# Kernel optimization log

Hardware: AMD Instinct MI355X
Metric: run time of the kernel (lower is better)

## Reference

```python
import jax, jax.numpy as jnp
import numpy as np

D_MODEL = 1024
NUM_HEADS = 16
DEPTH = D_MODEL // NUM_HEADS


def setup_inputs() -> dict:
    key = jax.random.key(0)
    ks = jax.random.split(key, 12)
    B, S = 4, 2048
    scale = 1.0 / np.sqrt(D_MODEL)
    inp = {
        "query": jax.random.normal(ks[0], (B, S, D_MODEL), jnp.float32),
        "key": jax.random.normal(ks[1], (B, S, D_MODEL), jnp.float32),
        "value": jax.random.normal(ks[2], (B, S, D_MODEL), jnp.float32),
        "mask": jnp.zeros((B, 1, 1, S), jnp.float32),  # 1.0 => masked position
        "wq": jax.random.normal(ks[3], (D_MODEL, D_MODEL), jnp.float32) * scale,
        "bq": jnp.zeros((D_MODEL,), jnp.float32),
        "wk": jax.random.normal(ks[4], (D_MODEL, D_MODEL), jnp.float32) * scale,
        "bk": jnp.zeros((D_MODEL,), jnp.float32),
        "wv": jax.random.normal(ks[5], (D_MODEL, D_MODEL), jnp.float32) * scale,
        "bv": jnp.zeros((D_MODEL,), jnp.float32),
        "wo": jax.random.normal(ks[6], (D_MODEL, D_MODEL), jnp.float32) * scale,
        "bo": jnp.zeros((D_MODEL,), jnp.float32),
    }
    return inp


def _split_heads(x, B):
    # (B, S, d_model) -> (B, H, S, depth)
    return x.reshape(B, -1, NUM_HEADS, DEPTH).transpose(0, 2, 1, 3)


def reference(query, key, value, mask, wq, bq, wk, bk, wv, bv, wo, bo):
    B, Sq, _ = query.shape
    q = _split_heads(query @ wq + bq, B)   # (B,H,Sq,dh)
    k = _split_heads(key @ wk + bk, B)     # (B,H,Sk,dh)
    v = _split_heads(value @ wv + bv, B)   # (B,H,Sk,dh)

    logits = jnp.einsum("bhqd,bhkd->bhqk", q, k) / jnp.sqrt(
        jnp.asarray(DEPTH, q.dtype))
    logits = logits + mask * (-1e9)
    attn = jax.nn.softmax(logits, axis=-1)
    ctx = jnp.einsum("bhqk,bhkd->bhqd", attn, v)
    ctx = ctx.transpose(0, 2, 1, 3).reshape(B, Sq, D_MODEL)
    return ctx @ wo + bo
```

## Files before the change

kernel.cpp:

```cpp
#include <hip/hip_runtime.h>
#include <stdint.h>


typedef unsigned short u16;
typedef __attribute__((ext_vector_type(8))) short bf16x8;
typedef __attribute__((ext_vector_type(4))) short bf16x4;
typedef __attribute__((ext_vector_type(4))) float f32x4;

#define LOG2E 1.4426950408889634f

__device__ __forceinline__ u16 f2bf(float f) {
  uint32_t u = __builtin_bit_cast(uint32_t, f);
  u += 0x7fffu + ((u >> 16) & 1u);
  return (u16)(u >> 16);
}
__device__ __forceinline__ uint32_t cvt_pk(float a, float b) {
  uint32_t r;
  asm("v_cvt_pk_bf16_f32 %0, %1, %2" : "=v"(r) : "v"(a), "v"(b));
  return r;
}
__device__ __forceinline__ void gload16(const u16* g, u16* l) {
  __builtin_amdgcn_global_load_lds(
      (const __attribute__((address_space(1))) uint32_t*)(const void*)g,
      (__attribute__((address_space(3))) uint32_t*)(void*)l, 16, 0, 0);
}
__device__ __forceinline__ f32x4 mfma16(bf16x4 a, bf16x4 b, f32x4 c) {
#if __has_builtin(__builtin_amdgcn_mfma_f32_16x16x16bf16_1k)
  return __builtin_amdgcn_mfma_f32_16x16x16bf16_1k(a, b, c, 0, 0, 0);
#else
  f32x4 d = c;
  asm volatile("v_mfma_f32_16x16x16_bf16 %0, %1, %2, %0"
               : "+v"(d) : "v"(a), "v"(b));
  return d;
#endif
}

__global__ __launch_bounds__(256) void convert_x(
    const float* __restrict__ X, u16* __restrict__ Xb)
{
  const size_t i = ((size_t)blockIdx.x * 256 + threadIdx.x) * 8;
  const float4 a = *(const float4*)(X + i);
  const float4 b = *(const float4*)(X + i + 4);
  uint4 o;
  o.x = cvt_pk(a.x, a.y); o.y = cvt_pk(a.z, a.w);
  o.z = cvt_pk(b.x, b.y); o.w = cvt_pk(b.z, b.w);
  *(uint4*)(Xb + i) = o;
}

__global__ __launch_bounds__(256) void prep_mask(
    const float* __restrict__ mask, float* __restrict__ M2)
{
  const int i = blockIdx.x * 256 + threadIdx.x;
  M2[i] = mask[i] * (-1.0e9f * LOG2E);
}

__global__ __launch_bounds__(256) void transpose_w(
    const float* __restrict__ W0, const float* __restrict__ W1,
    const float* __restrict__ W2, const float* __restrict__ W3,
    u16* __restrict__ Wt)
{
  const int z = blockIdx.z;
  const float* W = (z == 0) ? W0 : (z == 1) ? W1 : (z == 2) ? W2 : W3;
  u16* T = Wt + ((size_t)z << 20);
  const int n0 = blockIdx.x * 64, k0 = blockIdx.y * 64;
  const int tid = threadIdx.x;
  const int r = tid >> 4, c4 = (tid & 15) * 4;
  __shared__ float t[64][65];
#pragma unroll
  for (int j = 0; j < 4; ++j) {
    const int row = r + j * 16;
    const float4 v = *(const float4*)(W + (size_t)(k0 + row) * 1024 + n0 + c4);
    t[c4 + 0][row] = v.x; t[c4 + 1][row] = v.y;
    t[c4 + 2][row] = v.z; t[c4 + 3][row] = v.w;
  }
  __syncthreads();
#pragma unroll
  for (int j = 0; j < 4; ++j) {
    const int nrow = r + j * 16;
    uint2 o;
    o.x = cvt_pk(t[nrow][c4 + 0], t[nrow][c4 + 1]);
    o.y = cvt_pk(t[nrow][c4 + 2], t[nrow][c4 + 3]);
    *(uint2*)(T + (size_t)(n0 + nrow) * 1024 + k0 + c4) = o;
  }
}

__global__ __launch_bounds__(256) void gemm_proj(
    const u16* __restrict__ A, const u16* __restrict__ Wt,
    const float* __restrict__ Bi, u16* __restrict__ O16,
    float* __restrict__ O32, int mode)
{
  const int bid = blockIdx.x;
  const int nid = (bid & 7) * 64 + (bid >> 3);
  const int n0 = (nid & 7) * 128;
  const int m0 = (nid >> 3) * 128;
  const int tid = threadIdx.x;
  const int w = tid >> 6, l = tid & 63, lo = l & 15, hi = l >> 4;
  const int wr = w >> 1, wc = w & 1;

  __shared__ __align__(16) u16 As[128 * 32];
  __shared__ __align__(16) u16 Bs[128 * 32];

  const f32x4 fz = {0.f, 0.f, 0.f, 0.f};
  f32x4 acc[4][4];
#pragma unroll
  for (int m = 0; m < 4; ++m)
#pragma unroll
    for (int n = 0; n < 4; ++n) acc[m][n] = fz;

  const int srow = w * 32 + (l >> 2);
  const u16* ga = A  + (size_t)(m0 + srow) * 1024 + (l & 3) * 8;
  const u16* gb = Wt + (size_t)(n0 + srow) * 1024 + (l & 3) * 8;
  u16* lA0 = &As[w * 1024];  u16* lA1 = &As[w * 1024 + 512];
  u16* lB0 = &Bs[w * 1024];  u16* lB1 = &Bs[w * 1024 + 512];

  for (int k0 = 0; k0 < 1024; k0 += 32) {
    __syncthreads();
    gload16(ga,             lA0);
    gload16(ga + 16 * 1024, lA1);
    gload16(gb,             lB0);
    gload16(gb + 16 * 1024, lB1);
    ga += 32; gb += 32;
    __syncthreads();

    bf16x8 af[4], bf[4];
#pragma unroll
    for (int m = 0; m < 4; ++m)
      af[m] = *(const bf16x8*)&As[(wr * 64 + m * 16 + lo) * 32 + hi * 8];
#pragma unroll
    for (int n = 0; n < 4; ++n)
      bf[n] = *(const bf16x8*)&Bs[(wc * 64 + n * 16 + lo) * 32 + hi * 8];
#pragma unroll
    for (int m = 0; m < 4; ++m)
#pragma unroll
      for (int n = 0; n < 4; ++n)
        acc[m][n] = __builtin_amdgcn_mfma_f32_16x16x32_bf16(af[m], bf[n], acc[m][n], 0, 0, 0);
  }

#pragma unroll
  for (int m = 0; m < 4; ++m) {
#pragma unroll
    for (int n = 0; n < 4; ++n) {
      const int col = n0 + wc * 64 + n * 16 + lo;
      const float bc = Bi[col];
      const int h = col >> 6, d = col & 63;
#pragma unroll
      for (int i = 0; i < 4; ++i) {
        const int r = m0 + wr * 64 + m * 16 + hi * 4 + i;
        const int b = r >> 11, s = r & 2047;
        float v = acc[m][n][i] + bc;
        if (mode == 0) {
          v *= 0.125f * LOG2E;
          O16[((size_t)((b * 16 + h) * 2048 + s)) * 64 + d] = f2bf(v);
        } else if (mode == 1) {
          O16[((size_t)((b * 16 + h) * 2048 + s)) * 64 + d] = f2bf(v);
        } else if (mode == 2) {
          O16[((size_t)((b * 16 + h) * 64 + d)) * 2048 + s] = f2bf(v);
        } else {
          O32[(size_t)r * 1024 + col] = v;
        }
      }
    }
  }
}

__global__ __launch_bounds__(512, 4) void attn(
    const u16* __restrict__ Q, const u16* __restrict__ K,
    const u16* __restrict__ Vt, const float* __restrict__ M2,
    u16* __restrict__ Ctx)
{
  const int bid = blockIdx.x;
  const int nid = (bid & 7) * 128 + (bid >> 3);
  const int qt = nid & 15;
  const int bh = nid >> 4;
  const int b = bh >> 4, h = bh & 15;
  const int tid = threadIdx.x;
  const int w = tid >> 6, l = tid & 63, lo = l & 15, hi = l >> 4;

  __shared__ __align__(16) u16 Kl[2][64 * 64];
  __shared__ __align__(16) u16 Vl[2][64 * 64];
  __shared__ __align__(16) float Msk[2048];

  const u16* Qb = Q + (size_t)bh * (2048 * 64);
  const u16* Kb = K + (size_t)bh * (2048 * 64);
  const u16* Vb = Vt + (size_t)bh * (64 * 2048);

  *(float4*)&Msk[tid * 4] = *(const float4*)(M2 + (size_t)b * 2048 + tid * 4);

  const int qrow = qt * 128 + w * 16 + lo;
  const bf16x8 qa0 = *(const bf16x8*)(Qb + (size_t)qrow * 64 + hi * 8);
  const bf16x8 qa1 = *(const bf16x8*)(Qb + (size_t)qrow * 64 + 32 + hi * 8);

  const f32x4 fz = {0.f, 0.f, 0.f, 0.f};
  f32x4 o[4] = {fz, fz, fz, fz};
  f32x4 ol = fz;
  const short oneb = (short)0x3F80;
  const bf16x4 ones = {oneb, oneb, oneb, oneb};
  const int lo7 = lo & 7;

  const int row = tid >> 3;
  const int sl = (tid & 7) ^ (row & 7);
  const u16* gK = Kb + (size_t)row * 64 + sl * 8;
  const u16* gV = Vb + (size_t)row * 2048 + sl * 8;

#define STAGE(kt_, buf_)                                  \
  do {                                                    \
    gload16(gK + (size_t)(kt_) * 4096, &Kl[buf_][w * 512]); \
    gload16(gV + (kt_) * 64,           &Vl[buf_][w * 512]); \
  } while (0)

  STAGE(0, 0);
  __syncthreads();

  for (int kt = 0; kt < 32; ++kt) {
    const int cur = kt & 1;
    STAGE((kt + 1) & 31, cur ^ 1);
    asm volatile("s_waitcnt vmcnt(2)" ::: "memory");
    __builtin_amdgcn_s_barrier();

    const int kv0 = kt * 64;
    const u16* Kc = &Kl[cur][0];
    const u16* Vc = &Vl[cur][0];

    f32x4 st[4];
    __builtin_amdgcn_s_setprio(1);
#pragma unroll
    for (int f = 0; f < 4; ++f) {
      const int krow = (f * 16 + lo) * 64;
      const bf16x8 kb0 = *(const bf16x8*)&Kc[krow + ((hi ^ lo7) << 3)];
      const bf16x8 kb1 = *(const bf16x8*)&Kc[krow + (((4 + hi) ^ lo7) << 3)];
      const f32x4 c = *(const f32x4*)&Msk[kv0 + 16 * f + 4 * hi];
      f32x4 a = __builtin_amdgcn_mfma_f32_16x16x32_bf16(kb0, qa0, c, 0, 0, 0);
      st[f] = __builtin_amdgcn_mfma_f32_16x16x32_bf16(kb1, qa1, a, 0, 0, 0);
    }
    __builtin_amdgcn_s_setprio(0);

    union { uint32_t u[2]; bf16x4 v; } pa[4];
#pragma unroll
    for (int f = 0; f < 4; ++f) {
      const float p0 = exp2f(st[f][0]);
      const float p1 = exp2f(st[f][1]);
      const float p2 = exp2f(st[f][2]);
      const float p3 = exp2f(st[f][3]);
      pa[f].u[0] = cvt_pk(p0, p1);
      pa[f].u[1] = cvt_pk(p2, p3);
    }

    __builtin_amdgcn_s_setprio(1);
#pragma unroll
    for (int f = 0; f < 4; ++f) {
      ol = mfma16(pa[f].v, ones, ol);
#pragma unroll
      for (int nf = 0; nf < 4; ++nf) {
        const int vrow = (lo + 16 * nf) * 64;
        const int slot = (((2 * f + (hi >> 1)) ^ lo7) << 3) + ((hi & 1) << 2);
        const bf16x4 vb = *(const bf16x4*)&Vc[vrow + slot];
        o[nf] = mfma16(pa[f].v, vb, o[nf]);
      }
    }
    __builtin_amdgcn_s_setprio(0);

    asm volatile("s_waitcnt lgkmcnt(0)" ::: "memory");
    __builtin_amdgcn_s_barrier();
  }
#undef STAGE

  float invq[4];
#pragma unroll
  for (int i = 0; i < 4; ++i) invq[i] = 1.f / ol[i];
#pragma unroll
  for (int nf = 0; nf < 4; ++nf) {
#pragma unroll
    for (int i = 0; i < 4; ++i) {
      const int s = qt * 128 + w * 16 + hi * 4 + i;
      const int d = nf * 16 + lo;
      Ctx[((size_t)((b * 2048 + s) * 16 + h)) * 64 + d] = f2bf(o[nf][i] * invq[i]);
    }
  }
}

extern "C" void kernel_launch(void* const* d_in, const int* in_sizes, int n_in,
                              void* d_out, int out_size, void* d_ws, size_t ws_size,
                              hipStream_t stream) {
  const float* q_in = (const float*)d_in[0];
  const float* k_in = (const float*)d_in[1];
  const float* v_in = (const float*)d_in[2];
  const float* mask = (const float*)d_in[3];
  const float* wq = (const float*)d_in[4];
  const float* bq = (const float*)d_in[5];
  const float* wk = (const float*)d_in[6];
  const float* bk = (const float*)d_in[7];
  const float* wv = (const float*)d_in[8];
  const float* bv = (const float*)d_in[9];
  const float* wo = (const float*)d_in[10];
  const float* bo = (const float*)d_in[11];

  u16* ws  = (u16*)d_ws;
  u16* wtq = ws;
  u16* wtk = wtq + (1u << 20);
  u16* wtv = wtk + (1u << 20);
  u16* wto = wtv + (1u << 20);
  u16* Qb  = wto + (1u << 20);
  u16* Kb  = Qb + (size_t)8192 * 1024;
  u16* Vtb = Kb + (size_t)8192 * 1024;
  u16* xbf = Vtb + (size_t)8192 * 1024;
  u16* ctx = xbf;
  float* M2 = (float*)(xbf + (size_t)8192 * 1024);

  transpose_w<<<dim3(16, 16, 4), 256, 0, stream>>>(wq, wk, wv, wo, wtq);
  prep_mask<<<32, 256, 0, stream>>>(mask, M2);

  convert_x<<<4096, 256, 0, stream>>>(q_in, xbf);
  gemm_proj<<<512, 256, 0, stream>>>(xbf, wtq, bq, Qb, nullptr, 0);
  convert_x<<<4096, 256, 0, stream>>>(k_in, xbf);
  gemm_proj<<<512, 256, 0, stream>>>(xbf, wtk, bk, Kb, nullptr, 1);
  convert_x<<<4096, 256, 0, stream>>>(v_in, xbf);
  gemm_proj<<<512, 256, 0, stream>>>(xbf, wtv, bv, Vtb, nullptr, 2);

  attn<<<1024, 512, 0, stream>>>(Qb, Kb, Vtb, M2, ctx);

  gemm_proj<<<512, 256, 0, stream>>>(ctx, wto, bo, nullptr, (float*)d_out, 3);
}
```

Baseline: 281.2 us.

## Process two query row-tiles per wave in attention with 256-thread blocks

The attention kernel drops from 8 waves to 4 waves per block, and each wave now handles 32 query rows as two 16-row MFMA tiles. Each K/V fragment read from LDS is therefore reused across two tiles, which halves LDS read traffic per unit of MFMA work. Each thread now issues twice as many staging loads and holds twice as many accumulators. The cost is higher register pressure and fewer waves per block to hide latency.

Result: faster. 268.5 us (-4.5%).

```diff
diff --git a/kernel.cpp b/kernel.cpp
--- a/kernel.cpp
+++ b/kernel.cpp
@@ -163,7 +163,7 @@
   }
 }
 
-__global__ __launch_bounds__(512, 4) void attn(
+__global__ __launch_bounds__(256, 4) void attn(
     const u16* __restrict__ Q, const u16* __restrict__ K,
     const u16* __restrict__ Vt, const float* __restrict__ M2,
     u16* __restrict__ Ctx)
@@ -176,36 +176,48 @@
   const int tid = threadIdx.x;
   const int w = tid >> 6, l = tid & 63, lo = l & 15, hi = l >> 4;
 
-  __shared__ __align__(16) u16 Kl[2][64 * 64];
-  __shared__ __align__(16) u16 Vl[2][64 * 64];
+  __shared__ __align__(16) u16 Kl[2][4096];
+  __shared__ __align__(16) u16 Vl[2][4096];
   __shared__ __align__(16) float Msk[2048];
 
   const u16* Qb = Q + (size_t)bh * (2048 * 64);
   const u16* Kb = K + (size_t)bh * (2048 * 64);
   const u16* Vb = Vt + (size_t)bh * (64 * 2048);
 
-  *(float4*)&Msk[tid * 4] = *(const float4*)(M2 + (size_t)b * 2048 + tid * 4);
-
-  const int qrow = qt * 128 + w * 16 + lo;
-  const bf16x8 qa0 = *(const bf16x8*)(Qb + (size_t)qrow * 64 + hi * 8);
-  const bf16x8 qa1 = *(const bf16x8*)(Qb + (size_t)qrow * 64 + 32 + hi * 8);
+  {
+    const float* ms = M2 + (size_t)b * 2048 + tid * 8;
+    *(float4*)&Msk[tid * 8]     = *(const float4*)(ms);
+    *(float4*)&Msk[tid * 8 + 4] = *(const float4*)(ms + 4);
+  }
+
+  const int qrow0 = qt * 128 + w * 32 + lo;
+  const bf16x8 qa00 = *(const bf16x8*)(Qb + (size_t)qrow0 * 64 + hi * 8);
+  const bf16x8 qa01 = *(const bf16x8*)(Qb + (size_t)qrow0 * 64 + 32 + hi * 8);
+  const bf16x8 qa10 = *(const bf16x8*)(Qb + (size_t)(qrow0 + 16) * 64 + hi * 8);
+  const bf16x8 qa11 = *(const bf16x8*)(Qb + (size_t)(qrow0 + 16) * 64 + 32 + hi * 8);
 
   const f32x4 fz = {0.f, 0.f, 0.f, 0.f};
-  f32x4 o[4] = {fz, fz, fz, fz};
-  f32x4 ol = fz;
+  f32x4 o0[4] = {fz, fz, fz, fz};
+  f32x4 o1[4] = {fz, fz, fz, fz};
+  f32x4 ol0 = fz, ol1 = fz;
   const short oneb = (short)0x3F80;
   const bf16x4 ones = {oneb, oneb, oneb, oneb};
   const int lo7 = lo & 7;
 
-  const int row = tid >> 3;
-  const int sl = (tid & 7) ^ (row & 7);
-  const u16* gK = Kb + (size_t)row * 64 + sl * 8;
-  const u16* gV = Vb + (size_t)row * 2048 + sl * 8;
-
-#define STAGE(kt_, buf_)                                  \
-  do {                                                    \
-    gload16(gK + (size_t)(kt_) * 4096, &Kl[buf_][w * 512]); \
-    gload16(gV + (kt_) * 64,           &Vl[buf_][w * 512]); \
+  const int unitA = w * 64 + l;
+  const int rowA  = unitA >> 3;
+  const int slA   = (unitA & 7) ^ (rowA & 7);
+  const u16* gK = Kb + (size_t)rowA * 64 + slA * 8;
+  const u16* gV = Vb + (size_t)rowA * 2048 + slA * 8;
+
+#define STAGE(kt_, buf_)                                        \
+  do {                                                          \
+    const u16* gk_ = gK + (size_t)(kt_) * 4096;                 \
+    const u16* gv_ = gV + (kt_) * 64;                           \
+    gload16(gk_,             &Kl[buf_][w * 512]);               \
+    gload16(gk_ + 32 * 64,   &Kl[buf_][2048 + w * 512]);        \
+    gload16(gv_,             &Vl[buf_][w * 512]);               \
+    gload16(gv_ + 32 * 2048, &Vl[buf_][2048 + w * 512]);        \
   } while (0)
 
   STAGE(0, 0);
@@ -214,14 +226,14 @@
   for (int kt = 0; kt < 32; ++kt) {
     const int cur = kt & 1;
     STAGE((kt + 1) & 31, cur ^ 1);
-    asm volatile("s_waitcnt vmcnt(2)" ::: "memory");
+    asm volatile("s_waitcnt vmcnt(4)" ::: "memory");
     __builtin_amdgcn_s_barrier();
 
     const int kv0 = kt * 64;
     const u16* Kc = &Kl[cur][0];
     const u16* Vc = &Vl[cur][0];
 
-    f32x4 st[4];
+    f32x4 st0[4], st1[4];
     __builtin_amdgcn_s_setprio(1);
 #pragma unroll
     for (int f = 0; f < 4; ++f) {
@@ -229,32 +241,34 @@
       const bf16x8 kb0 = *(const bf16x8*)&Kc[krow + ((hi ^ lo7) << 3)];
       const bf16x8 kb1 = *(const bf16x8*)&Kc[krow + (((4 + hi) ^ lo7) << 3)];
       const f32x4 c = *(const f32x4*)&Msk[kv0 + 16 * f + 4 * hi];
-      f32x4 a = __builtin_amdgcn_mfma_f32_16x16x32_bf16(kb0, qa0, c, 0, 0, 0);
-      st[f] = __builtin_amdgcn_mfma_f32_16x16x32_bf16(kb1, qa1, a, 0, 0, 0);
+      f32x4 a0 = __builtin_amdgcn_mfma_f32_16x16x32_bf16(kb0, qa00, c, 0, 0, 0);
+      st0[f] = __builtin_amdgcn_mfma_f32_16x16x32_bf16(kb1, qa01, a0, 0, 0, 0);
+      f32x4 a1 = __builtin_amdgcn_mfma_f32_16x16x32_bf16(kb0, qa10, c, 0, 0, 0);
+      st1[f] = __builtin_amdgcn_mfma_f32_16x16x32_bf16(kb1, qa11, a1, 0, 0, 0);
     }
     __builtin_amdgcn_s_setprio(0);
 
-    union { uint32_t u[2]; bf16x4 v; } pa[4];
+    union { uint32_t u[2]; bf16x4 v; } pa0[4], pa1[4];
 #pragma unroll
     for (int f = 0; f < 4; ++f) {
-      const float p0 = exp2f(st[f][0]);
-      const float p1 = exp2f(st[f][1]);
-      const float p2 = exp2f(st[f][2]);
-      const float p3 = exp2f(st[f][3]);
-      pa[f].u[0] = cvt_pk(p0, p1);
-      pa[f].u[1] = cvt_pk(p2, p3);
+      pa0[f].u[0] = cvt_pk(exp2f(st0[f][0]), exp2f(st0[f][1]));
+      pa0[f].u[1] = cvt_pk(exp2f(st0[f][2]), exp2f(st0[f][3]));
+      pa1[f].u[0] = cvt_pk(exp2f(st1[f][0]), exp2f(st1[f][1]));
+      pa1[f].u[1] = cvt_pk(exp2f(st1[f][2]), exp2f(st1[f][3]));
     }
 
     __builtin_amdgcn_s_setprio(1);
 #pragma unroll
     for (int f = 0; f < 4; ++f) {
-      ol = mfma16(pa[f].v, ones, ol);
+      ol0 = mfma16(pa0[f].v, ones, ol0);
+      ol1 = mfma16(pa1[f].v, ones, ol1);
 #pragma unroll
       for (int nf = 0; nf < 4; ++nf) {
         const int vrow = (lo + 16 * nf) * 64;
         const int slot = (((2 * f + (hi >> 1)) ^ lo7) << 3) + ((hi & 1) << 2);
         const bf16x4 vb = *(const bf16x4*)&Vc[vrow + slot];
-        o[nf] = mfma16(pa[f].v, vb, o[nf]);
+        o0[nf] = mfma16(pa0[f].v, vb, o0[nf]);
+        o1[nf] = mfma16(pa1[f].v, vb, o1[nf]);
       }
     }
     __builtin_amdgcn_s_setprio(0);
@@ -264,16 +278,17 @@
   }
 #undef STAGE
 
-  float invq[4];
-#pragma unroll
-  for (int i = 0; i < 4; ++i) invq[i] = 1.f / ol[i];
+  float inv0[4], inv1[4];
+#pragma unroll
+  for (int i = 0; i < 4; ++i) { inv0[i] = 1.f / ol0[i]; inv1[i] = 1.f / ol1[i]; }
 #pragma unroll
   for (int nf = 0; nf < 4; ++nf) {
 #pragma unroll
     for (int i = 0; i < 4; ++i) {
-      const int s = qt * 128 + w * 16 + hi * 4 + i;
+      const int s0 = qt * 128 + w * 32 + hi * 4 + i;
       const int d = nf * 16 + lo;
-      Ctx[((size_t)((b * 2048 + s) * 16 + h)) * 64 + d] = f2bf(o[nf][i] * invq[i]);
+      Ctx[((size_t)((b * 2048 + s0) * 16 + h)) * 64 + d] = f2bf(o0[nf][i] * inv0[i]);
+      Ctx[((size_t)((b * 2048 + s0 + 16) * 16 + h)) * 64 + d] = f2bf(o1[nf][i] * inv1[i]);
     }
   }
 }
@@ -316,7 +331,7 @@
   convert_x<<<4096, 256, 0, stream>>>(v_in, xbf);
   gemm_proj<<<512, 256, 0, stream>>>(xbf, wtv, bv, Vtb, nullptr, 2);
 
-  attn<<<1024, 512, 0, stream>>>(Qb, Kb, Vtb, M2, ctx);
+  attn<<<1024, 256, 0, stream>>>(Qb, Kb, Vtb, M2, ctx);
 
   gemm_proj<<<512, 256, 0, stream>>>(ctx, wto, bo, nullptr, (float*)d_out, 3);
 }
```
